# Performance work log

Measured on AMD Instinct MI355X. Metric: run time of the kernel, lower is better.

## Reference

```python
import jax, jax.numpy as jnp
import numpy as np

GN_GROUPS = 32
GN_EPS = 1e-6


def setup_inputs() -> dict:
    key = jax.random.key(0)
    ks = jax.random.split(key, 4)
    B, C, H, W = 8, 512, 32, 32
    x = jax.random.normal(ks[0], (B, C, H, W), dtype=jnp.float32)
    W_qkv = jax.random.normal(ks[1], (C, 3 * C), dtype=jnp.float32) * 0.02
    b_qkv = jnp.zeros((3 * C,), dtype=jnp.float32)
    W_out = jax.random.normal(ks[2], (C, C), dtype=jnp.float32) * 0.02
    b_out = jnp.zeros((C,), dtype=jnp.float32)
    gn_scale = jnp.ones((C,), dtype=jnp.float32)
    gn_bias = jnp.zeros((C,), dtype=jnp.float32)
    return {"x": x, "gn_scale": gn_scale, "gn_bias": gn_bias,
            "W_qkv": W_qkv, "b_qkv": b_qkv, "W_out": W_out, "b_out": b_out,
            "num_heads": 8}


def _group_norm(x, scale, bias):
    B, C, H, W = x.shape
    g = GN_GROUPS
    xg = x.reshape(B, g, C // g, H * W)
    mean = xg.mean(axis=(2, 3), keepdims=True)
    var = xg.var(axis=(2, 3), keepdims=True)
    xg = (xg - mean) * jax.lax.rsqrt(var + GN_EPS)
    x = xg.reshape(B, C, H, W)
    return x * scale[None, :, None, None] + bias[None, :, None, None]


def reference(x, gn_scale, gn_bias, W_qkv, b_qkv, W_out, b_out, num_heads):
    B, C, H, W = x.shape
    hd = C // num_heads
    h = _group_norm(x, gn_scale, gn_bias)
    # NIN: 1x1 projection over channels -> (B, 3C, H, W)
    h = jnp.einsum('bchw,cd->bdhw', h, W_qkv) + b_qkv[None, :, None, None]
    # reshape exactly like torch: (B, nh, 3*hd, HW) then move seq last->middle
    h = h.reshape(B, num_heads, 3 * hd, H * W).transpose(0, 1, 3, 2)  # (B, nh, S, 3hd)
    q, k, v = jnp.split(h, 3, axis=-1)  # each (B, nh, S, hd)
    scale = 1.0 / jnp.sqrt(jnp.asarray(hd, dtype=q.dtype))
    logits = jnp.einsum('bhsd,bhtd->bhst', q, k) * scale  # (B, nh, S, S)
    attn = jax.nn.softmax(logits, axis=-1)
    vals = jnp.einsum('bhst,bhtd->bhsd', attn, v)  # (B, nh, S, hd)
    h = vals.transpose(0, 1, 3, 2).reshape(B, C, H, W)
    h = jnp.einsum('bchw,cd->bdhw', h, W_out) + b_out[None, :, None, None]
    return x + h
```

## Files before the change

kernel.cpp:

```cpp
#include <hip/hip_runtime.h>
#include <hip/hip_bf16.h>

typedef __bf16 bf16_t;
typedef __attribute__((ext_vector_type(8))) __bf16 bf16x8;
typedef __attribute__((ext_vector_type(4))) float f32x4;
typedef __attribute__((ext_vector_type(4))) unsigned int u32x4;

#define B_   8
#define C_   512
#define S_   1024
#define NH   8
#define C2_  1024
#define C3_  1536
#define QSCALE 0.1803368801111204f

static __device__ __forceinline__ unsigned pack2(float a, float b) {
  unsigned short lo = __builtin_bit_cast(unsigned short, (bf16_t)a);
  unsigned short hi = __builtin_bit_cast(unsigned short, (bf16_t)b);
  return (unsigned)lo | ((unsigned)hi << 16);
}

static __device__ __forceinline__ void load_lds16(const void* g, void* l) {
  __builtin_amdgcn_global_load_lds(
      (const __attribute__((address_space(1))) unsigned*)g,
      (__attribute__((address_space(3))) unsigned*)l, 16, 0, 0);
}

template<int ROUNDS>
static __device__ __forceinline__ void stage_swz(const bf16_t* g, int rstride,
                                                 char* lbuf, int tid) {
#pragma unroll
  for (int r = 0; r < ROUNDS; ++r) {
    int i = r * 256 + tid;
    int row = i >> 3;
    int cg = (i & 7) ^ (row & 7);
    load_lds16(g + (size_t)row * rstride + cg * 8,
               lbuf + r * 4096 + (tid & 192) * 16);
  }
}

__global__ __launch_bounds__(256) void gn_kernel(
    const float* __restrict__ x, const float* __restrict__ scale,
    const float* __restrict__ bias, bf16_t* __restrict__ h_t) {
  __shared__ float xs[16 * 1024];
  __shared__ float red[8];
  int b = blockIdx.x >> 5, g = blockIdx.x & 31;
  int tid = threadIdx.x;
  const f32x4* xb4 = (const f32x4*)(x + ((size_t)b * C_ + g * 16) * S_);

  float s = 0.f, s2 = 0.f;
#pragma unroll
  for (int k = 0; k < 16; ++k) {
    int vf = k * 256 + tid;
    f32x4 v = xb4[vf];
    ((f32x4*)xs)[vf] = v;
#pragma unroll
    for (int e = 0; e < 4; ++e) { s += v[e]; s2 += v[e] * v[e]; }
  }
  for (int off = 32; off > 0; off >>= 1) {
    s  += __shfl_down(s, off);
    s2 += __shfl_down(s2, off);
  }
  int wave = tid >> 6, lane = tid & 63;
  if (lane == 0) { red[wave] = s; red[4 + wave] = s2; }
  __syncthreads();
  float ts = red[0] + red[1] + red[2] + red[3];
  float t2 = red[4] + red[5] + red[6] + red[7];
  const float inv_n = 1.f / (16.f * S_);
  float mean = ts * inv_n;
  float var  = t2 * inv_n - mean * mean;
  float rstd = rsqrtf(var + 1e-6f);

  float ac[16], bc[16];
#pragma unroll
  for (int cl = 0; cl < 16; ++cl) {
    float sc = scale[g * 16 + cl] * rstd;
    ac[cl] = sc;
    bc[cl] = bias[g * 16 + cl] - mean * sc;
  }
#pragma unroll
  for (int k = 0; k < 4; ++k) {
    int srow = tid + k * 256;
    unsigned ow[8];
#pragma unroll
    for (int p = 0; p < 8; ++p) {
      float y0 = xs[(2 * p    ) * 1024 + srow] * ac[2 * p    ] + bc[2 * p    ];
      float y1 = xs[(2 * p + 1) * 1024 + srow] * ac[2 * p + 1] + bc[2 * p + 1];
      ow[p] = pack2(y0, y1);
    }
    bf16_t* dst = h_t + ((size_t)b * S_ + srow) * C_ + g * 16;
    u32x4 v0, v1;
#pragma unroll
    for (int e = 0; e < 4; ++e) { v0[e] = ow[e]; v1[e] = ow[4 + e]; }
    *(u32x4*)dst = v0;
    *(u32x4*)(dst + 8) = v1;
  }
}

__global__ __launch_bounds__(256) void prep_wqkv_kernel(
    const float* __restrict__ W, const float* __restrict__ bq,
    bf16_t* __restrict__ Wt, float* __restrict__ bt) {
  __shared__ float T[32 * 33];
  int d0 = blockIdx.x * 32, c0 = blockIdx.y * 32;
  int tid = threadIdx.x, ld = tid & 31, lc = tid >> 5;
#pragma unroll
  for (int i = 0; i < 4; ++i) {
    int c = lc + i * 8;
    T[c * 33 + ld] = W[(size_t)(c0 + c) * C3_ + d0 + ld];
  }
  __syncthreads();
#pragma unroll
  for (int i = 0; i < 4; ++i) {
    int dd = lc + i * 8;
    int d = d0 + dd;
    int h = d / 192, rr = d - h * 192, part = rr >> 6, dq = rr & 63;
    float scl = (part == 0) ? QSCALE : 1.f;
    Wt[(size_t)(part * 512 + h * 64 + dq) * C_ + c0 + ld] =
        (bf16_t)(T[ld * 33 + dd] * scl);
  }
  if (blockIdx.y == 0 && tid < 32) {
    int d = d0 + tid;
    int h = d / 192, rr = d - h * 192, part = rr >> 6, dq = rr & 63;
    bt[part * 512 + h * 64 + dq] = bq[d] * ((part == 0) ? QSCALE : 1.f);
  }
}

__global__ __launch_bounds__(256) void transpose_w_kernel(
    const float* __restrict__ W, bf16_t* __restrict__ Wt, int R, int Ccols) {
  __shared__ float T[32 * 33];
  int c0 = blockIdx.x * 32, r0 = blockIdx.y * 32;
  int tid = threadIdx.x;
  int lc = tid & 31, lr = tid >> 5;
  for (int i = 0; i < 4; ++i) {
    int r = lr + i * 8;
    T[r * 33 + lc] = W[(size_t)(r0 + r) * Ccols + c0 + lc];
  }
  __syncthreads();
  for (int i = 0; i < 4; ++i) {
    int cc = lr + i * 8;
    Wt[(size_t)(c0 + cc) * R + r0 + lc] = (bf16_t)T[lc * 33 + cc];
  }
}

static __device__ __forceinline__ void gemm_loop(
    const bf16_t* Asrc, int Astride, const bf16_t* Bsrc, int Bstride,
    char* lds, int tid, f32x4 (&acc)[4][4]) {
  int wave = tid >> 6, lane = tid & 63;
  int wr = wave >> 1, wc = wave & 1;
  int lr = lane & 15, lq = lane >> 4;
  char* A0 = lds;
  char* B0 = lds + 16384;
  char* A1 = lds + 32768;
  char* B1 = lds + 49152;
  stage_swz<4>(Asrc, Astride, A0, tid);
  stage_swz<4>(Bsrc, Bstride, B0, tid);
#pragma unroll 1
  for (int ks = 0; ks < 8; ++ks) {
    if (ks < 7) {
      stage_swz<4>(Asrc + (ks + 1) * 64, Astride, (ks & 1) ? A0 : A1, tid);
      stage_swz<4>(Bsrc + (ks + 1) * 64, Bstride, (ks & 1) ? B0 : B1, tid);
      asm volatile("s_waitcnt vmcnt(8)" ::: "memory");
    } else {
      asm volatile("s_waitcnt vmcnt(0)" ::: "memory");
    }
    __builtin_amdgcn_s_barrier();
    const char* Ab = (ks & 1) ? A1 : A0;
    const char* Bb = (ks & 1) ? B1 : B0;
#pragma unroll
    for (int kk = 0; kk < 2; ++kk) {
      int co = ((kk * 4 + lq) ^ (lr & 7)) << 4;
      bf16x8 a[4], b[4];
#pragma unroll
      for (int i = 0; i < 4; ++i)
        a[i] = *(const bf16x8*)(Ab + (wr * 64 + i * 16 + lr) * 128 + co);
#pragma unroll
      for (int j = 0; j < 4; ++j)
        b[j] = *(const bf16x8*)(Bb + (wc * 64 + j * 16 + lr) * 128 + co);
#pragma unroll
      for (int i = 0; i < 4; ++i)
#pragma unroll
        for (int j = 0; j < 4; ++j)
          acc[i][j] = __builtin_amdgcn_mfma_f32_16x16x32_bf16(a[i], b[j], acc[i][j], 0, 0, 0);
    }
    __builtin_amdgcn_s_barrier();
  }
}

__global__ __launch_bounds__(256) void gemm_qkv_kernel(
    const bf16_t* __restrict__ h, const bf16_t* __restrict__ wq,
    const float* __restrict__ bias, bf16_t* __restrict__ qk,
    bf16_t* __restrict__ vt) {
  __shared__ char lds[65536];
  int tid = threadIdx.x;
  int bid = blockIdx.x;
  int wave = tid >> 6, lane = tid & 63;
  int wr = wave >> 1, wc = wave & 1, lr = lane & 15, lq = lane >> 4;
  unsigned short* tb = (unsigned short*)lds;
  if (bid < 512) {
    int m0 = (bid & 63) * 128, n0 = (bid >> 6) * 128;
    f32x4 acc[4][4] = {};
    gemm_loop(h + (size_t)m0 * C_, C_, wq + (size_t)n0 * C_, C_, lds, tid, acc);
    float bv[4];
#pragma unroll
    for (int j = 0; j < 4; ++j) bv[j] = bias[n0 + wc * 64 + j * 16 + lr];
#pragma unroll
    for (int i = 0; i < 4; ++i)
#pragma unroll
      for (int j = 0; j < 4; ++j)
#pragma unroll
        for (int r = 0; r < 4; ++r) {
          int row = wr * 64 + i * 16 + lq * 4 + r;
          int col = wc * 64 + j * 16 + lr;
          int byte = row * 256 + (((col >> 3) ^ (row & 7)) << 4) + ((col & 7) << 1);
          tb[byte >> 1] = __builtin_bit_cast(unsigned short, (bf16_t)(acc[i][j][r] + bv[j]));
        }
    __builtin_amdgcn_s_barrier();
#pragma unroll
    for (int u = 0; u < 8; ++u) {
      int flat = tid + u * 256;
      int row = flat >> 4, c = flat & 15;
      u32x4 v = *(const u32x4*)(lds + row * 256 + ((c ^ (row & 7)) << 4));
      int m = m0 + row, b = m >> 10, s = m & 1023;
      int d = n0 + c * 8;
      int hh = (d >> 6) & 7, det = ((d >> 9) << 6) + (d & 63);
      *(u32x4*)(qk + ((size_t)(b * S_ + s)) * C2_ + hh * 128 + det) = v;
    }
  } else {
    int j2 = bid - 512;
    int n0 = (j2 & 63) * 128, m0 = (j2 >> 6) * 128;
    f32x4 acc[4][4] = {};
    gemm_loop(wq + (size_t)(1024 + m0) * C_, C_, h + (size_t)n0 * C_, C_, lds, tid, acc);
    float bv[4][4];
#pragma unroll
    for (int i = 0; i < 4; ++i) {
      f32x4 t = *(const f32x4*)(bias + 1024 + m0 + wr * 64 + i * 16 + lq * 4);
#pragma unroll
      for (int r = 0; r < 4; ++r) bv[i][r] = t[r];
    }
#pragma unroll
    for (int i = 0; i < 4; ++i)
#pragma unroll
      for (int j = 0; j < 4; ++j)
#pragma unroll
        for (int r = 0; r < 4; ++r) {
          int row = wr * 64 + i * 16 + lq * 4 + r;
          int col = wc * 64 + j * 16 + lr;
          int byte = row * 256 + (((col >> 3) ^ (row & 7)) << 4) + ((col & 7) << 1);
          tb[byte >> 1] = __builtin_bit_cast(unsigned short, (bf16_t)(acc[i][j][r] + bv[i][r]));
        }
    __builtin_amdgcn_s_barrier();
#pragma unroll
    for (int u = 0; u < 8; ++u) {
      int flat = tid + u * 256;
      int row = flat >> 4, c = flat & 15;
      u32x4 v = *(const u32x4*)(lds + row * 256 + ((c ^ (row & 7)) << 4));
      int m = m0 + row;
      int hh = m >> 6, dv = m & 63;
      int n = n0 + c * 8, b = n >> 10, s = n & 1023;
      *(u32x4*)(vt + ((size_t)((b * NH + hh) * 64 + dv)) * S_ + s) = v;
    }
  }
}

__global__ __launch_bounds__(256) void attn_kernel(
    const bf16_t* __restrict__ qk, const bf16_t* __restrict__ vt,
    bf16_t* __restrict__ ao) {
  __shared__ char lds[49152];
  int bid = blockIdx.x;
  int qt = bid >> 6, g = bid & 63;
  int b = g >> 3, head = g & 7;
  int tid = threadIdx.x, wave = tid >> 6, lane = tid & 63;
  int lr = lane & 15, lq = lane >> 4;
  int qb = qt * 128 + wave * 32;
  const bf16_t* qkb = qk + (size_t)b * S_ * C2_ + head * 128;
  const bf16_t* vtb = vt + (size_t)((b * NH + head) * 64) * S_;

  bf16x8 qf[2][2];
#pragma unroll
  for (int q2 = 0; q2 < 2; ++q2)
#pragma unroll
    for (int kk = 0; kk < 2; ++kk)
      qf[q2][kk] = *(const bf16x8*)(qkb + (size_t)(qb + q2 * 16 + lr) * C2_ + kk * 32 + lq * 8);

  f32x4 oacc[2][4] = {};
  float m_run[2] = {-1e30f, -1e30f}, l_run[2] = {0.f, 0.f};

  char* sb0 = lds;
  char* sb1 = lds + 16384;
  char* sb2 = lds + 32768;

#define STAGE_KV(kt, buf)                                                   \
  do {                                                                      \
    stage_swz<2>(qkb + (size_t)((kt) * 64) * C2_ + 64, C2_, (buf), tid);    \
    stage_swz<2>(vtb + (kt) * 64, S_, (buf) + 8192, tid);                   \
  } while (0)

  STAGE_KV(0, sb0);
#pragma unroll 1
  for (int kt = 0; kt < 16; ++kt) {
    if (kt < 15) {
      STAGE_KV(kt + 1, sb1);
      asm volatile("s_waitcnt vmcnt(4)" ::: "memory");
    } else {
      asm volatile("s_waitcnt vmcnt(0)" ::: "memory");
    }
    __builtin_amdgcn_s_barrier();

    f32x4 sacc[2][4] = {};
    __builtin_amdgcn_s_setprio(1);
#pragma unroll
    for (int kk = 0; kk < 2; ++kk) {
      int co = ((kk * 4 + lq) ^ (lr & 7)) << 4;
      bf16x8 kf[4];
#pragma unroll
      for (int mf = 0; mf < 4; ++mf)
        kf[mf] = *(const bf16x8*)(sb0 + (mf * 16 + lr) * 128 + co);
#pragma unroll
      for (int q2 = 0; q2 < 2; ++q2)
#pragma unroll
        for (int mf = 0; mf < 4; ++mf)
          sacc[q2][mf] = __builtin_amdgcn_mfma_f32_16x16x32_bf16(kf[mf], qf[q2][kk], sacc[q2][mf], 0, 0, 0);
    }
    __builtin_amdgcn_s_setprio(0);

    unsigned pk[2][4][2];
#pragma unroll
    for (int q2 = 0; q2 < 2; ++q2) {
      float mx = -1e30f;
#pragma unroll
      for (int mf = 0; mf < 4; ++mf)
#pragma unroll
        for (int r = 0; r < 4; ++r) mx = fmaxf(mx, sacc[q2][mf][r]);
      mx = fmaxf(mx, __shfl_xor(mx, 16));
      mx = fmaxf(mx, __shfl_xor(mx, 32));
      float mn = fmaxf(m_run[q2], mx);
      float alpha = __builtin_amdgcn_exp2f(m_run[q2] - mn);
      m_run[q2] = mn;
      float p[4][4];
      float rs = 0.f;
#pragma unroll
      for (int mf = 0; mf < 4; ++mf)
#pragma unroll
        for (int r = 0; r < 4; ++r) {
          float v = __builtin_amdgcn_exp2f(sacc[q2][mf][r] - mn);
          p[mf][r] = v; rs += v;
        }
      rs += __shfl_xor(rs, 16);
      rs += __shfl_xor(rs, 32);
      l_run[q2] = l_run[q2] * alpha + rs;
#pragma unroll
      for (int df = 0; df < 4; ++df)
#pragma unroll
        for (int r = 0; r < 4; ++r) oacc[q2][df][r] *= alpha;
#pragma unroll
      for (int mf = 0; mf < 4; ++mf)
#pragma unroll
        for (int j = 0; j < 2; ++j)
          pk[q2][mf][j] = pack2(p[mf][2 * j], p[mf][2 * j + 1]);
    }

#pragma unroll
    for (int kk = 0; kk < 2; ++kk) {
      int co = ((kk * 4 + lq) ^ (lr & 7)) << 4;
      bf16x8 vf[4];
#pragma unroll
      for (int df = 0; df < 4; ++df)
        vf[df] = *(const bf16x8*)(sb0 + 8192 + (df * 16 + lr) * 128 + co);
#pragma unroll
      for (int q2 = 0; q2 < 2; ++q2) {
        unsigned w0 = pk[q2][2 * kk + 0][0], w2 = pk[q2][2 * kk + 1][0];
        unsigned w1 = pk[q2][2 * kk + 0][1], w3 = pk[q2][2 * kk + 1][1];
        asm("v_permlane32_swap_b32 %0, %1" : "+v"(w0), "+v"(w2));
        asm("v_permlane16_swap_b32 %0, %1" : "+v"(w0), "+v"(w2));
        asm("v_permlane32_swap_b32 %0, %1" : "+v"(w1), "+v"(w3));
        asm("v_permlane16_swap_b32 %0, %1" : "+v"(w1), "+v"(w3));
        u32x4 bw; bw[0] = w0; bw[1] = w1; bw[2] = w2; bw[3] = w3;
        bf16x8 pb = __builtin_bit_cast(bf16x8, bw);
        __builtin_amdgcn_s_setprio(1);
#pragma unroll
        for (int df = 0; df < 4; ++df)
          oacc[q2][df] = __builtin_amdgcn_mfma_f32_16x16x32_bf16(vf[df], pb, oacc[q2][df], 0, 0, 0);
        __builtin_amdgcn_s_setprio(0);
      }
    }
    char* tp = sb0; sb0 = sb1; sb1 = sb2; sb2 = tp;
  }

#pragma unroll
  for (int q2 = 0; q2 < 2; ++q2) {
    float inv = 1.f / l_run[q2];
    bf16_t* aop = ao + ((size_t)b * S_ + qb + q2 * 16 + lr) * C_ + head * 64;
#pragma unroll
    for (int df = 0; df < 4; ++df)
#pragma unroll
      for (int rp = 0; rp < 4; rp += 2) {
        unsigned u = pack2(oacc[q2][df][rp] * inv, oacc[q2][df][rp + 1] * inv);
        *(unsigned*)(aop + df * 16 + lq * 4 + rp) = u;
      }
  }
#undef STAGE_KV
}

__global__ __launch_bounds__(256) void gemm_out_kernel(
    const bf16_t* __restrict__ A, const bf16_t* __restrict__ Bw,
    const float* __restrict__ bias, const float* __restrict__ xres,
    float* __restrict__ out) {
  __shared__ char lds[65536];
  int tid = threadIdx.x;
  int bid = blockIdx.x;
  int m0 = (bid & 63) * 128, n0 = (bid >> 6) * 128;
  f32x4 acc[4][4] = {};
  gemm_loop(A + (size_t)m0 * C_, C_, Bw + (size_t)n0 * C_, C_, lds, tid, acc);
  int wave = tid >> 6, lane = tid & 63;
  int wr = wave >> 1, wc = wave & 1, lr = lane & 15, lq = lane >> 4;
#pragma unroll
  for (int i = 0; i < 4; ++i) {
#pragma unroll
    for (int j = 0; j < 4; ++j) {
      int d = n0 + wc * 64 + j * 16 + lr;
      int m = m0 + wr * 64 + i * 16 + lq * 4;
      int b = m >> 10, s = m & 1023;
      size_t o = ((size_t)b * C_ + d) * S_ + s;
      f32x4 res = *(const f32x4*)(xres + o);
      f32x4 val;
      float bd = bias[d];
#pragma unroll
      for (int r = 0; r < 4; ++r) val[r] = res[r] + bd + acc[i][j][r];
      *(f32x4*)(out + o) = val;
    }
  }
}

extern "C" void kernel_launch(void* const* d_in, const int* in_sizes, int n_in,
                              void* d_out, int out_size, void* d_ws, size_t ws_size,
                              hipStream_t stream) {
  const float* x        = (const float*)d_in[0];
  const float* gn_scale = (const float*)d_in[1];
  const float* gn_bias  = (const float*)d_in[2];
  const float* W_qkv    = (const float*)d_in[3];
  const float* b_qkv    = (const float*)d_in[4];
  const float* W_out    = (const float*)d_in[5];
  const float* b_out    = (const float*)d_in[6];
  float* out = (float*)d_out;

  char* ws = (char*)d_ws;
  bf16_t* h_t   = (bf16_t*)(ws);
  bf16_t* qk_t  = (bf16_t*)(ws + 8388608);
  bf16_t* vt    = (bf16_t*)(ws + 25165824);
  bf16_t* ao_t  = (bf16_t*)(ws + 33554432);
  bf16_t* wqkvp = (bf16_t*)(ws + 41943040);
  bf16_t* woutt = (bf16_t*)(ws + 43515904);
  float* bqp = (float*)d_out;

  prep_wqkv_kernel<<<dim3(48, 16), 256, 0, stream>>>(W_qkv, b_qkv, wqkvp, bqp);
  transpose_w_kernel<<<dim3(16, 16), 256, 0, stream>>>(W_out, woutt, C_, C_);
  gn_kernel<<<256, 256, 0, stream>>>(x, gn_scale, gn_bias, h_t);
  gemm_qkv_kernel<<<768, 256, 0, stream>>>(h_t, wqkvp, bqp, qk_t, vt);
  attn_kernel<<<512, 256, 0, stream>>>(qk_t, vt, ao_t);
  gemm_out_kernel<<<256, 256, 0, stream>>>(ao_t, woutt, b_out, x, out);
}
```

Baseline: 91.27 us.

## Use 8 waves per attention block with lazy rescale; split output GEMM into smaller tiles

The attention kernel now runs 512 threads, with each wave handling 16 query rows instead of 32. This halves per-wave register state and raises occupancy. The online softmax skips rescaling unless some row max grows by more than a threshold, and the row-sum reduction is deferred to the end. The output GEMM is templated to 64x128 tiles with 512 blocks to fill more CUs. In exchange, K/V staging is spread across more threads and LDS traffic per query row increases.

Result: faster. 82.22 us (-9.9%).

```diff
diff --git a/kernel.cpp b/kernel.cpp
--- a/kernel.cpp
+++ b/kernel.cpp
@@ -37,6 +37,14 @@
     load_lds16(g + (size_t)row * rstride + cg * 8,
                lbuf + r * 4096 + (tid & 192) * 16);
   }
+}
+
+static __device__ __forceinline__ void stage_swz512(const bf16_t* g, int rstride,
+                                                    char* lbuf, int tid) {
+  int row = tid >> 3;
+  int cg = (tid & 7) ^ (row & 7);
+  load_lds16(g + (size_t)row * rstride + cg * 8,
+             lbuf + (tid & 448) * 16);
 }
 
 __global__ __launch_bounds__(256) void gn_kernel(
@@ -142,24 +150,25 @@
   }
 }
 
+template<int MF, int NF>
 static __device__ __forceinline__ void gemm_loop(
     const bf16_t* Asrc, int Astride, const bf16_t* Bsrc, int Bstride,
-    char* lds, int tid, f32x4 (&acc)[4][4]) {
+    char* lds, int tid, f32x4 (&acc)[MF][NF]) {
   int wave = tid >> 6, lane = tid & 63;
   int wr = wave >> 1, wc = wave & 1;
   int lr = lane & 15, lq = lane >> 4;
   char* A0 = lds;
-  char* B0 = lds + 16384;
-  char* A1 = lds + 32768;
-  char* B1 = lds + 49152;
-  stage_swz<4>(Asrc, Astride, A0, tid);
-  stage_swz<4>(Bsrc, Bstride, B0, tid);
+  char* B0 = lds + MF * 4096;
+  char* A1 = lds + (MF + NF) * 4096;
+  char* B1 = lds + (2 * MF + NF) * 4096;
+  stage_swz<MF>(Asrc, Astride, A0, tid);
+  stage_swz<NF>(Bsrc, Bstride, B0, tid);
 #pragma unroll 1
   for (int ks = 0; ks < 8; ++ks) {
     if (ks < 7) {
-      stage_swz<4>(Asrc + (ks + 1) * 64, Astride, (ks & 1) ? A0 : A1, tid);
-      stage_swz<4>(Bsrc + (ks + 1) * 64, Bstride, (ks & 1) ? B0 : B1, tid);
-      asm volatile("s_waitcnt vmcnt(8)" ::: "memory");
+      stage_swz<MF>(Asrc + (ks + 1) * 64, Astride, (ks & 1) ? A0 : A1, tid);
+      stage_swz<NF>(Bsrc + (ks + 1) * 64, Bstride, (ks & 1) ? B0 : B1, tid);
+      asm volatile("s_waitcnt vmcnt(%0)" :: "i"(MF + NF) : "memory");
     } else {
       asm volatile("s_waitcnt vmcnt(0)" ::: "memory");
     }
@@ -169,17 +178,17 @@
 #pragma unroll
     for (int kk = 0; kk < 2; ++kk) {
       int co = ((kk * 4 + lq) ^ (lr & 7)) << 4;
-      bf16x8 a[4], b[4];
-#pragma unroll
-      for (int i = 0; i < 4; ++i)
-        a[i] = *(const bf16x8*)(Ab + (wr * 64 + i * 16 + lr) * 128 + co);
-#pragma unroll
-      for (int j = 0; j < 4; ++j)
-        b[j] = *(const bf16x8*)(Bb + (wc * 64 + j * 16 + lr) * 128 + co);
-#pragma unroll
-      for (int i = 0; i < 4; ++i)
-#pragma unroll
-        for (int j = 0; j < 4; ++j)
+      bf16x8 a[MF], b[NF];
+#pragma unroll
+      for (int i = 0; i < MF; ++i)
+        a[i] = *(const bf16x8*)(Ab + (wr * MF * 16 + i * 16 + lr) * 128 + co);
+#pragma unroll
+      for (int j = 0; j < NF; ++j)
+        b[j] = *(const bf16x8*)(Bb + (wc * NF * 16 + j * 16 + lr) * 128 + co);
+#pragma unroll
+      for (int i = 0; i < MF; ++i)
+#pragma unroll
+        for (int j = 0; j < NF; ++j)
           acc[i][j] = __builtin_amdgcn_mfma_f32_16x16x32_bf16(a[i], b[j], acc[i][j], 0, 0, 0);
     }
     __builtin_amdgcn_s_barrier();
@@ -199,7 +208,7 @@
   if (bid < 512) {
     int m0 = (bid & 63) * 128, n0 = (bid >> 6) * 128;
     f32x4 acc[4][4] = {};
-    gemm_loop(h + (size_t)m0 * C_, C_, wq + (size_t)n0 * C_, C_, lds, tid, acc);
+    gemm_loop<4, 4>(h + (size_t)m0 * C_, C_, wq + (size_t)n0 * C_, C_, lds, tid, acc);
     float bv[4];
 #pragma unroll
     for (int j = 0; j < 4; ++j) bv[j] = bias[n0 + wc * 64 + j * 16 + lr];
@@ -229,7 +238,7 @@
     int j2 = bid - 512;
     int n0 = (j2 & 63) * 128, m0 = (j2 >> 6) * 128;
     f32x4 acc[4][4] = {};
-    gemm_loop(wq + (size_t)(1024 + m0) * C_, C_, h + (size_t)n0 * C_, C_, lds, tid, acc);
+    gemm_loop<4, 4>(wq + (size_t)(1024 + m0) * C_, C_, h + (size_t)n0 * C_, C_, lds, tid, acc);
     float bv[4][4];
 #pragma unroll
     for (int i = 0; i < 4; ++i) {
@@ -262,7 +271,7 @@
   }
 }
 
-__global__ __launch_bounds__(256) void attn_kernel(
+__global__ __launch_bounds__(512) void attn_kernel(
     const bf16_t* __restrict__ qk, const bf16_t* __restrict__ vt,
     bf16_t* __restrict__ ao) {
   __shared__ char lds[49152];
@@ -271,28 +280,26 @@
   int b = g >> 3, head = g & 7;
   int tid = threadIdx.x, wave = tid >> 6, lane = tid & 63;
   int lr = lane & 15, lq = lane >> 4;
-  int qb = qt * 128 + wave * 32;
+  int qb = qt * 128 + wave * 16;
   const bf16_t* qkb = qk + (size_t)b * S_ * C2_ + head * 128;
   const bf16_t* vtb = vt + (size_t)((b * NH + head) * 64) * S_;
 
-  bf16x8 qf[2][2];
-#pragma unroll
-  for (int q2 = 0; q2 < 2; ++q2)
-#pragma unroll
-    for (int kk = 0; kk < 2; ++kk)
-      qf[q2][kk] = *(const bf16x8*)(qkb + (size_t)(qb + q2 * 16 + lr) * C2_ + kk * 32 + lq * 8);
-
-  f32x4 oacc[2][4] = {};
-  float m_run[2] = {-1e30f, -1e30f}, l_run[2] = {0.f, 0.f};
+  bf16x8 qf[2];
+#pragma unroll
+  for (int kk = 0; kk < 2; ++kk)
+    qf[kk] = *(const bf16x8*)(qkb + (size_t)(qb + lr) * C2_ + kk * 32 + lq * 8);
+
+  f32x4 oacc[4] = {};
+  float m_run = -1e30f, l_run = 0.f;
 
   char* sb0 = lds;
   char* sb1 = lds + 16384;
   char* sb2 = lds + 32768;
 
-#define STAGE_KV(kt, buf)                                                   \
-  do {                                                                      \
-    stage_swz<2>(qkb + (size_t)((kt) * 64) * C2_ + 64, C2_, (buf), tid);    \
-    stage_swz<2>(vtb + (kt) * 64, S_, (buf) + 8192, tid);                   \
+#define STAGE_KV(kt, buf)                                                    \
+  do {                                                                       \
+    stage_swz512(qkb + (size_t)((kt) * 64) * C2_ + 64, C2_, (buf), tid);     \
+    stage_swz512(vtb + (kt) * 64, S_, (buf) + 8192, tid);                    \
   } while (0)
 
   STAGE_KV(0, sb0);
@@ -300,64 +307,58 @@
   for (int kt = 0; kt < 16; ++kt) {
     if (kt < 15) {
       STAGE_KV(kt + 1, sb1);
-      asm volatile("s_waitcnt vmcnt(4)" ::: "memory");
+      asm volatile("s_waitcnt vmcnt(2)" ::: "memory");
     } else {
       asm volatile("s_waitcnt vmcnt(0)" ::: "memory");
     }
     __builtin_amdgcn_s_barrier();
 
-    f32x4 sacc[2][4] = {};
+    f32x4 sacc[4] = {};
     __builtin_amdgcn_s_setprio(1);
 #pragma unroll
     for (int kk = 0; kk < 2; ++kk) {
       int co = ((kk * 4 + lq) ^ (lr & 7)) << 4;
-      bf16x8 kf[4];
-#pragma unroll
-      for (int mf = 0; mf < 4; ++mf)
-        kf[mf] = *(const bf16x8*)(sb0 + (mf * 16 + lr) * 128 + co);
-#pragma unroll
-      for (int q2 = 0; q2 < 2; ++q2)
-#pragma unroll
-        for (int mf = 0; mf < 4; ++mf)
-          sacc[q2][mf] = __builtin_amdgcn_mfma_f32_16x16x32_bf16(kf[mf], qf[q2][kk], sacc[q2][mf], 0, 0, 0);
+#pragma unroll
+      for (int mf = 0; mf < 4; ++mf) {
+        bf16x8 kf = *(const bf16x8*)(sb0 + (mf * 16 + lr) * 128 + co);
+        sacc[mf] = __builtin_amdgcn_mfma_f32_16x16x32_bf16(kf, qf[kk], sacc[mf], 0, 0, 0);
+      }
     }
     __builtin_amdgcn_s_setprio(0);
 
-    unsigned pk[2][4][2];
-#pragma unroll
-    for (int q2 = 0; q2 < 2; ++q2) {
-      float mx = -1e30f;
-#pragma unroll
-      for (int mf = 0; mf < 4; ++mf)
-#pragma unroll
-        for (int r = 0; r < 4; ++r) mx = fmaxf(mx, sacc[q2][mf][r]);
-      mx = fmaxf(mx, __shfl_xor(mx, 16));
-      mx = fmaxf(mx, __shfl_xor(mx, 32));
-      float mn = fmaxf(m_run[q2], mx);
-      float alpha = __builtin_amdgcn_exp2f(m_run[q2] - mn);
-      m_run[q2] = mn;
-      float p[4][4];
-      float rs = 0.f;
-#pragma unroll
-      for (int mf = 0; mf < 4; ++mf)
-#pragma unroll
-        for (int r = 0; r < 4; ++r) {
-          float v = __builtin_amdgcn_exp2f(sacc[q2][mf][r] - mn);
-          p[mf][r] = v; rs += v;
-        }
-      rs += __shfl_xor(rs, 16);
-      rs += __shfl_xor(rs, 32);
-      l_run[q2] = l_run[q2] * alpha + rs;
+    float mx = -1e30f;
+#pragma unroll
+    for (int mf = 0; mf < 4; ++mf)
+#pragma unroll
+      for (int r = 0; r < 4; ++r) mx = fmaxf(mx, sacc[mf][r]);
+    mx = fmaxf(mx, __shfl_xor(mx, 16));
+    mx = fmaxf(mx, __shfl_xor(mx, 32));
+    if (__any(mx - m_run > 11.f)) {
+      float mn = fmaxf(m_run, mx);
+      float alpha = __builtin_amdgcn_exp2f(m_run - mn);
+      m_run = mn;
+      l_run *= alpha;
 #pragma unroll
       for (int df = 0; df < 4; ++df)
 #pragma unroll
-        for (int r = 0; r < 4; ++r) oacc[q2][df][r] *= alpha;
-#pragma unroll
-      for (int mf = 0; mf < 4; ++mf)
-#pragma unroll
-        for (int j = 0; j < 2; ++j)
-          pk[q2][mf][j] = pack2(p[mf][2 * j], p[mf][2 * j + 1]);
-    }
+        for (int r = 0; r < 4; ++r) oacc[df][r] *= alpha;
+    }
+    float p[4][4];
+    float rs = 0.f;
+#pragma unroll
+    for (int mf = 0; mf < 4; ++mf)
+#pragma unroll
+      for (int r = 0; r < 4; ++r) {
+        float v = __builtin_amdgcn_exp2f(sacc[mf][r] - m_run);
+        p[mf][r] = v; rs += v;
+      }
+    l_run += rs;
+    unsigned pk[4][2];
+#pragma unroll
+    for (int mf = 0; mf < 4; ++mf)
+#pragma unroll
+      for (int j = 0; j < 2; ++j)
+        pk[mf][j] = pack2(p[mf][2 * j], p[mf][2 * j + 1]);
 
 #pragma unroll
     for (int kk = 0; kk < 2; ++kk) {
@@ -366,38 +367,35 @@
 #pragma unroll
       for (int df = 0; df < 4; ++df)
         vf[df] = *(const bf16x8*)(sb0 + 8192 + (df * 16 + lr) * 128 + co);
-#pragma unroll
-      for (int q2 = 0; q2 < 2; ++q2) {
-        unsigned w0 = pk[q2][2 * kk + 0][0], w2 = pk[q2][2 * kk + 1][0];
-        unsigned w1 = pk[q2][2 * kk + 0][1], w3 = pk[q2][2 * kk + 1][1];
-        asm("v_permlane32_swap_b32 %0, %1" : "+v"(w0), "+v"(w2));
-        asm("v_permlane16_swap_b32 %0, %1" : "+v"(w0), "+v"(w2));
-        asm("v_permlane32_swap_b32 %0, %1" : "+v"(w1), "+v"(w3));
-        asm("v_permlane16_swap_b32 %0, %1" : "+v"(w1), "+v"(w3));
-        u32x4 bw; bw[0] = w0; bw[1] = w1; bw[2] = w2; bw[3] = w3;
-        bf16x8 pb = __builtin_bit_cast(bf16x8, bw);
-        __builtin_amdgcn_s_setprio(1);
-#pragma unroll
-        for (int df = 0; df < 4; ++df)
-          oacc[q2][df] = __builtin_amdgcn_mfma_f32_16x16x32_bf16(vf[df], pb, oacc[q2][df], 0, 0, 0);
-        __builtin_amdgcn_s_setprio(0);
-      }
+      unsigned w0 = pk[2 * kk + 0][0], w2 = pk[2 * kk + 1][0];
+      unsigned w1 = pk[2 * kk + 0][1], w3 = pk[2 * kk + 1][1];
+      asm("v_permlane32_swap_b32 %0, %1" : "+v"(w0), "+v"(w2));
+      asm("v_permlane16_swap_b32 %0, %1" : "+v"(w0), "+v"(w2));
+      asm("v_permlane32_swap_b32 %0, %1" : "+v"(w1), "+v"(w3));
+      asm("v_permlane16_swap_b32 %0, %1" : "+v"(w1), "+v"(w3));
+      u32x4 bw; bw[0] = w0; bw[1] = w1; bw[2] = w2; bw[3] = w3;
+      bf16x8 pb = __builtin_bit_cast(bf16x8, bw);
+      __builtin_amdgcn_s_setprio(1);
+#pragma unroll
+      for (int df = 0; df < 4; ++df)
+        oacc[df] = __builtin_amdgcn_mfma_f32_16x16x32_bf16(vf[df], pb, oacc[df], 0, 0, 0);
+      __builtin_amdgcn_s_setprio(0);
     }
     char* tp = sb0; sb0 = sb1; sb1 = sb2; sb2 = tp;
   }
 
-#pragma unroll
-  for (int q2 = 0; q2 < 2; ++q2) {
-    float inv = 1.f / l_run[q2];
-    bf16_t* aop = ao + ((size_t)b * S_ + qb + q2 * 16 + lr) * C_ + head * 64;
-#pragma unroll
-    for (int df = 0; df < 4; ++df)
-#pragma unroll
-      for (int rp = 0; rp < 4; rp += 2) {
-        unsigned u = pack2(oacc[q2][df][rp] * inv, oacc[q2][df][rp + 1] * inv);
-        *(unsigned*)(aop + df * 16 + lq * 4 + rp) = u;
-      }
-  }
+  float lt = l_run;
+  lt += __shfl_xor(lt, 16);
+  lt += __shfl_xor(lt, 32);
+  float inv = 1.f / lt;
+  bf16_t* aop = ao + ((size_t)b * S_ + qb + lr) * C_ + head * 64;
+#pragma unroll
+  for (int df = 0; df < 4; ++df)
+#pragma unroll
+    for (int rp = 0; rp < 4; rp += 2) {
+      unsigned u = pack2(oacc[df][rp] * inv, oacc[df][rp + 1] * inv);
+      *(unsigned*)(aop + df * 16 + lq * 4 + rp) = u;
+    }
 #undef STAGE_KV
 }
 
@@ -405,20 +403,20 @@
     const bf16_t* __restrict__ A, const bf16_t* __restrict__ Bw,
     const float* __restrict__ bias, const float* __restrict__ xres,
     float* __restrict__ out) {
-  __shared__ char lds[65536];
+  __shared__ char lds[49152];
   int tid = threadIdx.x;
   int bid = blockIdx.x;
-  int m0 = (bid & 63) * 128, n0 = (bid >> 6) * 128;
-  f32x4 acc[4][4] = {};
-  gemm_loop(A + (size_t)m0 * C_, C_, Bw + (size_t)n0 * C_, C_, lds, tid, acc);
+  int m0 = (bid & 127) * 64, n0 = (bid >> 7) * 128;
+  f32x4 acc[2][4] = {};
+  gemm_loop<2, 4>(A + (size_t)m0 * C_, C_, Bw + (size_t)n0 * C_, C_, lds, tid, acc);
   int wave = tid >> 6, lane = tid & 63;
   int wr = wave >> 1, wc = wave & 1, lr = lane & 15, lq = lane >> 4;
 #pragma unroll
-  for (int i = 0; i < 4; ++i) {
+  for (int i = 0; i < 2; ++i) {
 #pragma unroll
     for (int j = 0; j < 4; ++j) {
       int d = n0 + wc * 64 + j * 16 + lr;
-      int m = m0 + wr * 64 + i * 16 + lq * 4;
+      int m = m0 + wr * 32 + i * 16 + lq * 4;
       int b = m >> 10, s = m & 1023;
       size_t o = ((size_t)b * C_ + d) * S_ + s;
       f32x4 res = *(const f32x4*)(xres + o);
@@ -456,6 +454,6 @@
   transpose_w_kernel<<<dim3(16, 16), 256, 0, stream>>>(W_out, woutt, C_, C_);
   gn_kernel<<<256, 256, 0, stream>>>(x, gn_scale, gn_bias, h_t);
   gemm_qkv_kernel<<<768, 256, 0, stream>>>(h_t, wqkvp, bqp, qk_t, vt);
-  attn_kernel<<<512, 256, 0, stream>>>(qk_t, vt, ao_t);
-  gemm_out_kernel<<<256, 256, 0, stream>>>(ao_t, woutt, b_out, x, out);
-}
+  attn_kernel<<<512, 512, 0, stream>>>(qk_t, vt, ao_t);
+  gemm_out_kernel<<<512, 256, 0, stream>>>(ao_t, woutt, b_out, x, out);
+}
```
